# Performance work log

Hardware: AMD Instinct MI355X
Metric: run time of the kernel (lower is better)

Reference implementation:

```python
import jax, jax.numpy as jnp
import numpy as np
import math

B, T, C, H, ORDER = 2, 192, 512, 8, 3
HS = C // H  # head_size = 64


def setup_inputs() -> dict:
    key = jax.random.key(0)
    ks = jax.random.split(key, 12)
    init = lambda k, shape: (0.02 * jax.random.normal(k, shape, jnp.float32))
    return {
        "x0": jax.random.normal(ks[0], (B, T, C), jnp.float32),
        "x1": jax.random.normal(ks[1], (B, T, C), jnp.float32),
        "x2": jax.random.normal(ks[2], (B, T, C), jnp.float32),
        # per-head, per-modality Linear(C -> HS): weights (H, ORDER, HS, C), biases (H, ORDER, HS)
        "qw": init(ks[3], (H, ORDER, HS, C)), "qb": init(ks[4], (H, ORDER, HS)),
        "kw": init(ks[5], (H, ORDER, HS, C)), "kb": init(ks[6], (H, ORDER, HS)),
        "vw": init(ks[7], (H, ORDER, HS, C)), "vb": init(ks[8], (H, ORDER, HS)),
        # output projection Linear(C -> C)
        "cw": init(ks[9], (C, C)), "cb": init(ks[10], (C,)),
    }


def _proj(x, w, b):
    # x: (B,T,C), w: (H,HS,C), b: (H,HS) -> (B,H,T,HS)
    return jnp.einsum("btc,hdc->bhtd", x, w) + b[None, :, None, :]


def reference(x0, x1, x2, qw, qb, kw, kb, vw, vb, cw, cb):
    # order=3: query factor from x0, key factors from x1,x2, value factors from x1,x2
    Q0 = _proj(x0, qw[:, 0], qb[:, 0])  # (B,H,T0,HS)
    K1 = _proj(x1, kw[:, 1], kb[:, 1])  # (B,H,T1,HS)
    K2 = _proj(x2, kw[:, 2], kb[:, 2])  # (B,H,T2,HS)
    V1 = _proj(x1, vw[:, 1], vb[:, 1])  # (B,H,T1,HS)
    V2 = _proj(x2, vw[:, 2], vb[:, 2])  # (B,H,T2,HS)

    scale = 1.0 / math.sqrt(HS)
    # order-3 attention tensor: A[b,h,i,j,k] = sum_d Q0*K1*K2
    A = jnp.einsum("bhid,bhjd,bhkd->bhijk", Q0, K1, K2) * scale
    b, h, t0, t1, t2 = A.shape
    # softmax over the flattened (j,k) key dims, as in the torch code
    A = jax.nn.softmax(A.reshape(b, h, t0, t1 * t2), axis=-1).reshape(b, h, t0, t1, t2)
    # contract with outer-product-merged V: merged_V[b,j,k,d] = V1[b,j,d]*V2[b,k,d]
    Y = jnp.einsum("bhijk,bhjd,bhkd->bhid", A, V1, V2)  # (B,H,T0,HS)
    out = jnp.transpose(Y, (0, 2, 1, 3)).reshape(b, t0, h * HS)  # stack heads -> (B,T0,C)
    return out @ cw.T + cb
```

## Files before the change

kernel.cpp:

```cpp
#include <hip/hip_runtime.h>

typedef float f4v __attribute__((ext_vector_type(4)));
typedef _Float16 h2v __attribute__((ext_vector_type(2)));
typedef _Float16 h4v __attribute__((ext_vector_type(4)));
typedef _Float16 h8v __attribute__((ext_vector_type(8)));
typedef __fp16 g4 __attribute__((ext_vector_type(4)));
typedef __fp16 g8 __attribute__((ext_vector_type(8)));
typedef unsigned short u16;
typedef unsigned int u32;

#define SPLIT 8
#define ESC 0.18033688011112042f

__device__ __forceinline__ h2v pkh(float lo, float hi) {
  return __builtin_bit_cast(h2v, __builtin_amdgcn_cvt_pkrtz(lo, hi));
}
__device__ __forceinline__ f4v mfma_k32(h8v a, h8v b, f4v c) {
  return __builtin_amdgcn_mfma_f32_16x16x32_f16(
      __builtin_bit_cast(g8, a), __builtin_bit_cast(g8, b), c, 0, 0, 0);
}
__device__ __forceinline__ f4v mfma_k16(h4v a, h4v b, f4v c) {
  return __builtin_amdgcn_mfma_f32_16x16x16f16(
      __builtin_bit_cast(g4, a), __builtin_bit_cast(g4, b), c, 0, 0, 0);
}

__global__ __launch_bounds__(256) void prep_kernel(
    const float* __restrict__ x0, const float* __restrict__ x1,
    const float* __restrict__ x2,
    const float* __restrict__ qw, const float* __restrict__ kw,
    const float* __restrict__ vw,
    u16* __restrict__ xh, u16* __restrict__ wh) {
  int i = blockIdx.x * 256 + threadIdx.x;
  const int total = 1474560;
  for (; i < total; i += gridDim.x * 256) {
    const float* s; int off; u16* d;
    if (i < 294912) {
      int seg = i / 98304;
      s = seg == 0 ? x0 : seg == 1 ? x1 : x2;
      off = i - seg * 98304;
      d = xh + seg * 196608;
    } else {
      int j = i - 294912;
      int seg = j / 393216;
      s = seg == 0 ? qw : seg == 1 ? kw : vw;
      off = j - seg * 393216;
      d = wh + seg * 786432;
    }
    float2 v = *(const float2*)(s + (long)off * 2);
    *(u32*)(d + (long)off * 2) = __builtin_bit_cast(u32, pkh(v.x, v.y));
  }
}

__global__ __launch_bounds__(256) void proj_kernel(
    const u16* __restrict__ xh, const u16* __restrict__ wh,
    const float* __restrict__ qb, const float* __restrict__ kb,
    const float* __restrict__ vb,
    u16* __restrict__ Q0h, u16* __restrict__ K1h, float* __restrict__ V1f,
    u16* __restrict__ K2b, u16* __restrict__ V2b) {
  int g = blockIdx.x * 4 + (threadIdx.x >> 6);
  int lane = threadIdx.x & 63;
  int l15 = lane & 15, quad = lane >> 4;
  int slot = g / 768;
  int rem = g - slot * 768;
  int bh = rem / 48;
  int r2 = rem - bh * 48;
  int tt = r2 >> 2, dt = r2 & 3;
  int b = bh >> 3, h = bh & 7;

  int xsel, o, wsel;
  const float* bias;
  float* outf = nullptr; u16* outb = nullptr;
  switch (slot) {
    case 0: xsel = 0; o = 0; wsel = 0; bias = qb; outb = Q0h; break;
    case 1: xsel = 1; o = 1; wsel = 1; bias = kb; outb = K1h; break;
    case 2: xsel = 2; o = 2; wsel = 1; bias = kb; outb = K2b; break;
    case 3: xsel = 1; o = 1; wsel = 2; bias = vb; outf = V1f; break;
    default: xsel = 2; o = 2; wsel = 2; bias = vb; outb = V2b; break;
  }
  const u16* xp = xh + (long)xsel * 196608 +
                  ((long)(b * 192 + tt * 16 + l15)) * 512;
  const u16* wp = wh + (long)wsel * 786432 +
                  ((long)((h * 3 + o) * 64 + dt * 16 + l15)) * 512;
  bias += (h * 3 + o) * 64 + dt * 16;

  f4v acc = {0.f, 0.f, 0.f, 0.f};
#pragma unroll 4
  for (int kc = 0; kc < 16; ++kc) {
    h8v a = *(const h8v*)(wp + kc * 32 + quad * 8);
    h8v bf = *(const h8v*)(xp + kc * 32 + quad * 8);
    acc = mfma_k32(a, bf, acc);
  }

  float4 b4 = *(const float4*)(bias + quad * 4);
  int t = tt * 16 + l15;
  int d = dt * 16 + quad * 4;
  long base = ((long)(bh * 192 + t)) * 64 + d;
  float o0 = acc[0] + b4.x, o1 = acc[1] + b4.y;
  float o2 = acc[2] + b4.z, o3 = acc[3] + b4.w;
  if (slot == 0) { o0 *= ESC; o1 *= ESC; o2 *= ESC; o3 *= ESC; }
  if (outf) {
    float4 st = {o0, o1, o2, o3};
    *(float4*)(outf + base) = st;
  } else {
    uint2 st = {__builtin_bit_cast(u32, pkh(o0, o1)),
                __builtin_bit_cast(u32, pkh(o2, o3))};
    *(uint2*)(outb + base) = st;
  }
}

__global__ __launch_bounds__(256, 4) void attn_kernel(
    const u16* __restrict__ Q0h, const u16* __restrict__ K1h,
    const float* __restrict__ V1f, const u16* __restrict__ K2b,
    const u16* __restrict__ V2b, float* __restrict__ Op,
    float* __restrict__ lp) {
  __shared__ __align__(16) char smem[25856];
  int bx = blockIdx.x;
  int sp = bx / 192;
  int rem = bx - sp * 192;
  int bh = rem / 12;
  int itile = rem - bh * 12;
  int i0 = itile * 16;
  int js = sp * 24;
  int tid = threadIdx.x;
  int wave = tid >> 6;
  int lane = tid & 63;
  int l15 = lane & 15;
  int quad = lane >> 4;

  u16* K1s = (u16*)smem;
  float* V1s = (float*)(smem + 3072);

  u32 kreg0, kreg1, kreg2;
  float2 vreg0, vreg1, vreg2;
  {
    const u32* ksrc = (const u32*)(K1h + (bh * 192 + js) * 64);
    kreg0 = ksrc[tid]; kreg1 = ksrc[256 + tid]; kreg2 = ksrc[512 + tid];
    const float2* vsrc2 = (const float2*)(V1f + (bh * 192 + js) * 64);
    vreg0 = vsrc2[tid]; vreg1 = vsrc2[256 + tid]; vreg2 = vsrc2[512 + tid];
  }

  u16* V2T = (u16*)smem;
  {
    const u32* vsrc = (const u32*)V2b + bh * 6144;
#pragma unroll
    for (int r = 0; r < 24; ++r) {
      int idx = r * 256 + tid;
      int k = idx >> 5, d2 = idx & 31;
      u32 v = vsrc[idx];
      V2T[(d2 * 2) * 202 + k] = (u16)v;
      V2T[(d2 * 2 + 1) * 202 + k] = (u16)(v >> 16);
    }
  }
  h8v k2f[3][2];
#pragma unroll
  for (int nt = 0; nt < 3; ++nt)
#pragma unroll
    for (int ks = 0; ks < 2; ++ks)
      k2f[nt][ks] = *(const h8v*)(K2b +
          (bh * 192 + wave * 48 + nt * 16 + l15) * 64 + ks * 32 + quad * 8);
  const u16* qq = Q0h + (bh * 192 + i0 + l15) * 64 + quad * 8;
  h8v qh0 = *(const h8v*)qq;
  h8v qh1 = *(const h8v*)(qq + 32);
  __syncthreads();
  h8v v2g0[4]; h4v v2g1[4];
#pragma unroll
  for (int dt = 0; dt < 4; ++dt) {
    const char* p = smem + (dt * 16 + l15) * 404 + wave * 96 + quad * 8;
    union { h8v v; u32 w[4]; } u0;
    u0.w[0] = *(const u32*)p;        u0.w[1] = *(const u32*)(p + 4);
    u0.w[2] = *(const u32*)(p + 32); u0.w[3] = *(const u32*)(p + 36);
    v2g0[dt] = u0.v;
    union { h4v v; u32 w[2]; } u1;
    u1.w[0] = *(const u32*)(p + 64); u1.w[1] = *(const u32*)(p + 68);
    v2g1[dt] = u1.v;
  }
  __syncthreads();
  ((u32*)K1s)[tid] = kreg0;
  ((u32*)K1s)[256 + tid] = kreg1;
  ((u32*)K1s)[512 + tid] = kreg2;
  ((float2*)V1s)[tid] = vreg0;
  ((float2*)V1s)[256 + tid] = vreg1;
  ((float2*)V1s)[512 + tid] = vreg2;
  __syncthreads();

  f4v Oacc[4] = {};
  float lsum = 0.f;
  const f4v z = {0.f, 0.f, 0.f, 0.f};

#pragma unroll 1
  for (int j = 0; j < 24; ++j) {
    h8v c0 = *(const h8v*)(K1s + j * 64 + quad * 8);
    h8v c1 = *(const h8v*)(K1s + j * 64 + 32 + quad * 8);
    h8v B0 = qh0 * c0, B1 = qh1 * c1;
    f4v s0 = mfma_k32(k2f[0][0], B0, z);
    f4v s1 = mfma_k32(k2f[1][0], B0, z);
    f4v s2 = mfma_k32(k2f[2][0], B0, z);
    s0 = mfma_k32(k2f[0][1], B1, s0);
    s1 = mfma_k32(k2f[1][1], B1, s1);
    s2 = mfma_k32(k2f[2][1], B1, s2);
    float p[12];
#pragma unroll
    for (int r = 0; r < 4; ++r) {
      p[r] = __builtin_amdgcn_exp2f(s0[r]);
      p[4 + r] = __builtin_amdgcn_exp2f(s1[r]);
      p[8 + r] = __builtin_amdgcn_exp2f(s2[r]);
    }
    lsum += (((p[0] + p[1]) + (p[2] + p[3])) + ((p[4] + p[5]) + (p[6] + p[7]))) +
            ((p[8] + p[9]) + (p[10] + p[11]));
    union { h8v v; h2v h[4]; } pa0;
    pa0.h[0] = pkh(p[0], p[1]);  pa0.h[1] = pkh(p[2], p[3]);
    pa0.h[2] = pkh(p[4], p[5]);  pa0.h[3] = pkh(p[6], p[7]);
    union { h4v v; h2v h[2]; } pa1;
    pa1.h[0] = pkh(p[8], p[9]);  pa1.h[1] = pkh(p[10], p[11]);
    float v1r0 = V1s[j * 64 + l15];
    float v1r1 = V1s[j * 64 + 16 + l15];
    float v1r2 = V1s[j * 64 + 32 + l15];
    float v1r3 = V1s[j * 64 + 48 + l15];
#pragma unroll
    for (int dt = 0; dt < 4; ++dt) {
      f4v w = mfma_k32(pa0.v, v2g0[dt], z);
      w = mfma_k16(pa1.v, v2g1[dt], w);
      float v1x = dt == 0 ? v1r0 : dt == 1 ? v1r1 : dt == 2 ? v1r2 : v1r3;
      Oacc[dt][0] = fmaf(v1x, w[0], Oacc[dt][0]);
      Oacc[dt][1] = fmaf(v1x, w[1], Oacc[dt][1]);
      Oacc[dt][2] = fmaf(v1x, w[2], Oacc[dt][2]);
      Oacc[dt][3] = fmaf(v1x, w[3], Oacc[dt][3]);
    }
  }

  __syncthreads();
  float* ored = (float*)smem;
  float* lred = (float*)(smem + 16384);
  float* ow = ored + wave * 1024;
#pragma unroll
  for (int dt = 0; dt < 4; ++dt)
#pragma unroll
    for (int r = 0; r < 4; ++r)
      ow[(quad * 4 + r) * 64 + dt * 16 + l15] = Oacc[dt][r];
  lsum += __shfl_xor(lsum, 16);
  lsum += __shfl_xor(lsum, 32);
  if (quad == 0) lred[wave * 16 + l15] = lsum;
  __syncthreads();
  f4v s = *(const f4v*)(ored + tid * 4);
  s += *(const f4v*)(ored + 1024 + tid * 4);
  s += *(const f4v*)(ored + 2048 + tid * 4);
  s += *(const f4v*)(ored + 3072 + tid * 4);
  *(f4v*)(Op + ((long)(sp * 16 + bh) * 192 + i0) * 64 + tid * 4) = s;
  if (tid < 16)
    lp[(sp * 16 + bh) * 192 + i0 + tid] =
        lred[tid] + lred[16 + tid] + lred[32 + tid] + lred[48 + tid];
}

__global__ __launch_bounds__(256) void outproj_kernel(
    const float* __restrict__ Op, const float* __restrict__ lp,
    const float* __restrict__ cw, const float* __restrict__ cb,
    float* __restrict__ out) {
  __shared__ float xs[32][20];
  __shared__ float wsh[32][68];
  __shared__ float linv[8][16];
  int bx = blockIdx.x;
  int mt = bx >> 3, nt = bx & 7;
  int m0 = mt * 16;
  int b = m0 / 192;
  int t0 = m0 - b * 192;
  int n0 = nt * 64;
  int tid = threadIdx.x;

  if (tid < 128) {
    int h = tid >> 4, ml = tid & 15;
    float s = 0.f;
#pragma unroll
    for (int sp = 0; sp < SPLIT; ++sp)
      s += lp[(sp * 16 + b * 8 + h) * 192 + t0 + ml];
    linv[h][ml] = 1.0f / s;
  }

  int mA = tid >> 3, clA = (tid & 7) * 4;
  int nB0 = tid >> 3, nB1 = (256 + tid) >> 3;
  int m = tid >> 4, nq = tid & 15;
  float acc[4] = {};

  float4 pA[SPLIT];
  float4 pW0, pW1;
  {
    if (tid < 128) {
#pragma unroll
      for (int sp = 0; sp < SPLIT; ++sp)
        pA[sp] = *(const float4*)(
            Op + (long)((sp * 16 + b * 8) * 192 + t0 + mA) * 64 + clA);
    }
    pW0 = *(const float4*)(cw + (long)(n0 + nB0) * 512 + clA);
    pW1 = *(const float4*)(cw + (long)(n0 + nB1) * 512 + clA);
  }
  __syncthreads();

  for (int kc = 0; kc < 16; ++kc) {
    int h = kc >> 1;
    if (tid < 128) {
      float4 s = pA[0];
#pragma unroll
      for (int sp = 1; sp < SPLIT; ++sp) {
        s.x += pA[sp].x; s.y += pA[sp].y; s.z += pA[sp].z; s.w += pA[sp].w;
      }
      float li = linv[h][mA];
      xs[clA][mA] = s.x * li; xs[clA + 1][mA] = s.y * li;
      xs[clA + 2][mA] = s.z * li; xs[clA + 3][mA] = s.w * li;
    }
    wsh[clA][nB0] = pW0.x; wsh[clA + 1][nB0] = pW0.y;
    wsh[clA + 2][nB0] = pW0.z; wsh[clA + 3][nB0] = pW0.w;
    wsh[clA][nB1] = pW1.x; wsh[clA + 1][nB1] = pW1.y;
    wsh[clA + 2][nB1] = pW1.z; wsh[clA + 3][nB1] = pW1.w;
    __syncthreads();
    if (kc < 15) {
      int h2 = (kc + 1) >> 1, d2 = ((kc + 1) & 1) * 32;
      if (tid < 128) {
#pragma unroll
        for (int sp = 0; sp < SPLIT; ++sp)
          pA[sp] = *(const float4*)(
              Op + (long)((sp * 16 + b * 8 + h2) * 192 + t0 + mA) * 64 + d2 +
              clA);
      }
      pW0 = *(const float4*)(cw + (long)(n0 + nB0) * 512 + h2 * 64 + d2 + clA);
      pW1 = *(const float4*)(cw + (long)(n0 + nB1) * 512 + h2 * 64 + d2 + clA);
    }
#pragma unroll
    for (int c = 0; c < 32; ++c) {
      float a = xs[c][m];
      float4 bv = *(const float4*)&wsh[c][nq * 4];
      acc[0] += a * bv.x; acc[1] += a * bv.y;
      acc[2] += a * bv.z; acc[3] += a * bv.w;
    }
    __syncthreads();
  }

  float4 bias = *(const float4*)(cb + n0 + nq * 4);
  float4 st;
  st.x = acc[0] + bias.x;
  st.y = acc[1] + bias.y;
  st.z = acc[2] + bias.z;
  st.w = acc[3] + bias.w;
  *(float4*)(out + (long)(b * 192 + t0 + m) * 512 + n0 + nq * 4) = st;
}

extern "C" void kernel_launch(void* const* d_in, const int* in_sizes, int n_in,
                              void* d_out, int out_size, void* d_ws, size_t ws_size,
                              hipStream_t stream) {
  const float* x0 = (const float*)d_in[0];
  const float* x1 = (const float*)d_in[1];
  const float* x2 = (const float*)d_in[2];
  const float* qw = (const float*)d_in[3];
  const float* qb = (const float*)d_in[4];
  const float* kw = (const float*)d_in[5];
  const float* kb = (const float*)d_in[6];
  const float* vw = (const float*)d_in[7];
  const float* vb = (const float*)d_in[8];
  const float* cw = (const float*)d_in[9];
  const float* cb = (const float*)d_in[10];
  float* out = (float*)d_out;

  char* ws = (char*)d_ws;
  u16* Q0h = (u16*)(ws + 0);
  u16* K1h = (u16*)(ws + 393216);
  float* V1f = (float*)(ws + 786432);
  u16* K2b = (u16*)(ws + 1572864);
  u16* V2b = (u16*)(ws + 1966080);
  float* Op = (float*)(ws + 2359296);
  float* lp = (float*)(ws + 2359296 + (size_t)SPLIT * 786432);
  u16* xh = (u16*)(ws + 9437184);
  u16* wh = (u16*)(ws + 9437184 + 1179648);

  prep_kernel<<<1440, 256, 0, stream>>>(x0, x1, x2, qw, kw, vw, xh, wh);
  proj_kernel<<<960, 256, 0, stream>>>(xh, wh, qb, kb, vb,
                                       Q0h, K1h, V1f, K2b, V2b);
  attn_kernel<<<SPLIT * 192, 256, 0, stream>>>(Q0h, K1h, V1f, K2b, V2b,
                                               Op, lp);
  outproj_kernel<<<192, 256, 0, stream>>>(Op, lp, cw, cb, out);
}
```

Baseline: 146.5 us.

## Split output projection into fp16 combine pass and MFMA-based GEMM

Replaces the fp32 shared-memory output projection with two steps. A combine kernel reduces the split-K partial outputs, normalizes them by the softmax denominators and writes fp16 rows. A new outproj kernel then computes the projection with 16x16x32 f16 MFMA instructions directly from global memory. The cw weight is converted to fp16 in the existing prep kernel. This trades one extra kernel launch and fp16 rounding of the activations and weights for matrix-core throughput and removes the LDS staging and syncs.

```diff
diff --git a/kernel.cpp b/kernel.cpp
--- a/kernel.cpp
+++ b/kernel.cpp
@@ -28,10 +28,10 @@
     const float* __restrict__ x0, const float* __restrict__ x1,
     const float* __restrict__ x2,
     const float* __restrict__ qw, const float* __restrict__ kw,
-    const float* __restrict__ vw,
-    u16* __restrict__ xh, u16* __restrict__ wh) {
+    const float* __restrict__ vw, const float* __restrict__ cw,
+    u16* __restrict__ xh, u16* __restrict__ wh, u16* __restrict__ cwh) {
   int i = blockIdx.x * 256 + threadIdx.x;
-  const int total = 1474560;
+  const int total = 1605632;
   for (; i < total; i += gridDim.x * 256) {
     const float* s; int off; u16* d;
     if (i < 294912) {
@@ -39,12 +39,14 @@
       s = seg == 0 ? x0 : seg == 1 ? x1 : x2;
       off = i - seg * 98304;
       d = xh + seg * 196608;
-    } else {
+    } else if (i < 1474560) {
       int j = i - 294912;
       int seg = j / 393216;
       s = seg == 0 ? qw : seg == 1 ? kw : vw;
       off = j - seg * 393216;
       d = wh + seg * 786432;
+    } else {
+      s = cw; off = i - 1474560; d = cwh;
     }
     float2 v = *(const float2*)(s + (long)off * 2);
     *(u32*)(d + (long)off * 2) = __builtin_bit_cast(u32, pkh(v.x, v.y));
@@ -251,95 +253,49 @@
         lred[tid] + lred[16 + tid] + lred[32 + tid] + lred[48 + tid];
 }
 
+__global__ __launch_bounds__(256) void combine_kernel(
+    const float* __restrict__ Op, const float* __restrict__ lp,
+    u16* __restrict__ xh2) {
+  int idx = blockIdx.x * 256 + threadIdx.x;
+  int row = idx >> 8;
+  int cp = idx & 255;
+  int b = row / 192, t = row - b * 192;
+  int c = cp * 2;
+  int h = c >> 6, d = c & 63;
+  float sx = 0.f, sy = 0.f, l = 0.f;
+#pragma unroll
+  for (int sp = 0; sp < SPLIT; ++sp) {
+    int rowp = (sp * 16 + b * 8 + h) * 192 + t;
+    float2 v = *(const float2*)(Op + (long)rowp * 64 + d);
+    sx += v.x; sy += v.y;
+    l += lp[rowp];
+  }
+  float li = 1.0f / l;
+  *(u32*)(xh2 + (long)row * 512 + c) =
+      __builtin_bit_cast(u32, pkh(sx * li, sy * li));
+}
+
 __global__ __launch_bounds__(256) void outproj_kernel(
-    const float* __restrict__ Op, const float* __restrict__ lp,
-    const float* __restrict__ cw, const float* __restrict__ cb,
-    float* __restrict__ out) {
-  __shared__ float xs[32][20];
-  __shared__ float wsh[32][68];
-  __shared__ float linv[8][16];
-  int bx = blockIdx.x;
-  int mt = bx >> 3, nt = bx & 7;
-  int m0 = mt * 16;
-  int b = m0 / 192;
-  int t0 = m0 - b * 192;
-  int n0 = nt * 64;
-  int tid = threadIdx.x;
-
-  if (tid < 128) {
-    int h = tid >> 4, ml = tid & 15;
-    float s = 0.f;
-#pragma unroll
-    for (int sp = 0; sp < SPLIT; ++sp)
-      s += lp[(sp * 16 + b * 8 + h) * 192 + t0 + ml];
-    linv[h][ml] = 1.0f / s;
-  }
-
-  int mA = tid >> 3, clA = (tid & 7) * 4;
-  int nB0 = tid >> 3, nB1 = (256 + tid) >> 3;
-  int m = tid >> 4, nq = tid & 15;
-  float acc[4] = {};
-
-  float4 pA[SPLIT];
-  float4 pW0, pW1;
-  {
-    if (tid < 128) {
-#pragma unroll
-      for (int sp = 0; sp < SPLIT; ++sp)
-        pA[sp] = *(const float4*)(
-            Op + (long)((sp * 16 + b * 8) * 192 + t0 + mA) * 64 + clA);
-    }
-    pW0 = *(const float4*)(cw + (long)(n0 + nB0) * 512 + clA);
-    pW1 = *(const float4*)(cw + (long)(n0 + nB1) * 512 + clA);
-  }
-  __syncthreads();
-
+    const u16* __restrict__ xh2, const u16* __restrict__ cwh,
+    const float* __restrict__ cb, float* __restrict__ out) {
+  int g = blockIdx.x * 4 + (threadIdx.x >> 6);
+  int lane = threadIdx.x & 63;
+  int l15 = lane & 15, quad = lane >> 4;
+  int mt = g >> 5, nt = g & 31;
+  const u16* ap = cwh + ((long)(nt * 16 + l15)) * 512;
+  const u16* bp = xh2 + ((long)(mt * 16 + l15)) * 512;
+  f4v acc = {0.f, 0.f, 0.f, 0.f};
+#pragma unroll 4
   for (int kc = 0; kc < 16; ++kc) {
-    int h = kc >> 1;
-    if (tid < 128) {
-      float4 s = pA[0];
-#pragma unroll
-      for (int sp = 1; sp < SPLIT; ++sp) {
-        s.x += pA[sp].x; s.y += pA[sp].y; s.z += pA[sp].z; s.w += pA[sp].w;
-      }
-      float li = linv[h][mA];
-      xs[clA][mA] = s.x * li; xs[clA + 1][mA] = s.y * li;
-      xs[clA + 2][mA] = s.z * li; xs[clA + 3][mA] = s.w * li;
-    }
-    wsh[clA][nB0] = pW0.x; wsh[clA + 1][nB0] = pW0.y;
-    wsh[clA + 2][nB0] = pW0.z; wsh[clA + 3][nB0] = pW0.w;
-    wsh[clA][nB1] = pW1.x; wsh[clA + 1][nB1] = pW1.y;
-    wsh[clA + 2][nB1] = pW1.z; wsh[clA + 3][nB1] = pW1.w;
-    __syncthreads();
-    if (kc < 15) {
-      int h2 = (kc + 1) >> 1, d2 = ((kc + 1) & 1) * 32;
-      if (tid < 128) {
-#pragma unroll
-        for (int sp = 0; sp < SPLIT; ++sp)
-          pA[sp] = *(const float4*)(
-              Op + (long)((sp * 16 + b * 8 + h2) * 192 + t0 + mA) * 64 + d2 +
-              clA);
-      }
-      pW0 = *(const float4*)(cw + (long)(n0 + nB0) * 512 + h2 * 64 + d2 + clA);
-      pW1 = *(const float4*)(cw + (long)(n0 + nB1) * 512 + h2 * 64 + d2 + clA);
-    }
-#pragma unroll
-    for (int c = 0; c < 32; ++c) {
-      float a = xs[c][m];
-      float4 bv = *(const float4*)&wsh[c][nq * 4];
-      acc[0] += a * bv.x; acc[1] += a * bv.y;
-      acc[2] += a * bv.z; acc[3] += a * bv.w;
-    }
-    __syncthreads();
-  }
-
-  float4 bias = *(const float4*)(cb + n0 + nq * 4);
-  float4 st;
-  st.x = acc[0] + bias.x;
-  st.y = acc[1] + bias.y;
-  st.z = acc[2] + bias.z;
-  st.w = acc[3] + bias.w;
-  *(float4*)(out + (long)(b * 192 + t0 + m) * 512 + n0 + nq * 4) = st;
+    h8v a = *(const h8v*)(ap + kc * 32 + quad * 8);
+    h8v bf = *(const h8v*)(bp + kc * 32 + quad * 8);
+    acc = mfma_k32(a, bf, acc);
+  }
+  float4 b4 = *(const float4*)(cb + nt * 16 + quad * 4);
+  int t = mt * 16 + l15;
+  long base = (long)t * 512 + nt * 16 + quad * 4;
+  float4 st = {acc[0] + b4.x, acc[1] + b4.y, acc[2] + b4.z, acc[3] + b4.w};
+  *(float4*)(out + base) = st;
 }
 
 extern "C" void kernel_launch(void* const* d_in, const int* in_sizes, int n_in,
@@ -367,12 +323,16 @@
   float* Op = (float*)(ws + 2359296);
   float* lp = (float*)(ws + 2359296 + (size_t)SPLIT * 786432);
   u16* xh = (u16*)(ws + 9437184);
-  u16* wh = (u16*)(ws + 9437184 + 1179648);
-
-  prep_kernel<<<1440, 256, 0, stream>>>(x0, x1, x2, qw, kw, vw, xh, wh);
+  u16* wh = (u16*)(ws + 10616832);
+  u16* cwh = (u16*)(ws + 15335424);
+  u16* xh2 = (u16*)(ws + 15859712);
+
+  prep_kernel<<<1440, 256, 0, stream>>>(x0, x1, x2, qw, kw, vw, cw,
+                                        xh, wh, cwh);
   proj_kernel<<<960, 256, 0, stream>>>(xh, wh, qb, kb, vb,
                                        Q0h, K1h, V1f, K2b, V2b);
   attn_kernel<<<SPLIT * 192, 256, 0, stream>>>(Q0h, K1h, V1f, K2b, V2b,
                                                Op, lp);
-  outproj_kernel<<<192, 256, 0, stream>>>(Op, lp, cw, cb, out);
-}
+  combine_kernel<<<384, 256, 0, stream>>>(Op, lp, xh2);
+  outproj_kernel<<<192, 256, 0, stream>>>(xh2, cwh, cb, out);
+}
```

Result: faster. 139.9 us (-4.5%).
